# Kernel tuning notes

Hardware: AMD Instinct MI355X
Metric: run time of the kernel (lower is better)

## Reference

```python
import jax, jax.numpy as jnp
import numpy as np

BITS = 4
N_PACK = 8  # 32-bit container / 4-bit values
GROUP_SIZE = 128
MASK = (1 << BITS) - 1  # 0xF


def setup_inputs() -> dict:
    key = jax.random.key(0)
    k1, k2, k3, k4, k5 = jax.random.split(key, 5)
    in_f, out_f = 4096, 4096
    tokens = 8192
    n_groups = in_f // GROUP_SIZE
    x = jax.random.normal(k1, (tokens, in_f), dtype=jnp.float32)
    qweight = jax.random.randint(k2, (in_f // N_PACK, out_f), 0, 2147483647, dtype=jnp.int32)
    qzeros = jax.random.randint(k3, (n_groups, out_f // N_PACK), 0, 2147483647, dtype=jnp.int32)
    scales = jax.random.uniform(k4, (n_groups, out_f), dtype=jnp.float32) * 0.01 + 1e-3
    bias = jax.random.normal(k5, (out_f,), dtype=jnp.float32)
    return {"x": x, "qweight": qweight, "qzeros": qzeros, "scales": scales, "bias": bias}


def _unpack_rows(q):
    # q: [in/8, out] int32 -> [in, out] nibbles (unpack along dim 0)
    shifts = (jnp.arange(N_PACK, dtype=jnp.int32) * BITS)  # [8]
    w = (q[:, None, :] >> shifts[None, :, None]) & MASK    # [in/8, 8, out]
    return w.reshape(-1, q.shape[1])                       # [in, out]


def _unpack_cols(q):
    # q: [G, out/8] int32 -> [G, out] nibbles (unpack along dim 1)
    shifts = (jnp.arange(N_PACK, dtype=jnp.int32) * BITS)
    z = (q[:, :, None] >> shifts[None, None, :]) & MASK    # [G, out/8, 8]
    return z.reshape(q.shape[0], -1)                       # [G, out]


def reference(x, qweight, qzeros, scales, bias):
    in_f = qweight.shape[0] * N_PACK
    int_w = _unpack_rows(qweight)                 # [in, out] uint nibbles
    zp = _unpack_cols(qzeros) + 1                 # optimum format: zp was stored as zp-1
    g = jnp.arange(in_f) // GROUP_SIZE            # group index per input channel
    # dequantize: W[i, j] = (int_w[i,j] - zp[g(i), j]) * scales[g(i), j]
    W = (int_w.astype(jnp.float32) - zp[g].astype(jnp.float32)) * scales[g]
    return x @ W + bias
```

## Files before the change

kernel.cpp:

```cpp
#include <hip/hip_runtime.h>
#include <hip/hip_bf16.h>
#include <stdint.h>

typedef __bf16 bf8 __attribute__((ext_vector_type(8)));
typedef float  f4  __attribute__((ext_vector_type(4)));

__device__ __forceinline__ unsigned f2bf(float f) {
  union { float f; unsigned u; } v; v.f = f;
  return (v.u + 0x7FFFu + ((v.u >> 16) & 1u)) >> 16;
}

__device__ __forceinline__ void gload_lds16(const void* g, void* l) {
  __builtin_amdgcn_global_load_lds(
      (const __attribute__((address_space(1))) void*)(uintptr_t)g,
      (__attribute__((address_space(3))) void*)(uint32_t)(uintptr_t)l,
      16, 0, 0);
}

__global__ void cvt_x(const float4* __restrict__ x, uint4* __restrict__ xb, int n16) {
  int i = blockIdx.x * blockDim.x + threadIdx.x;
  if (i >= n16) return;
  float4 f0 = x[2 * i], f1 = x[2 * i + 1];
  uint4 w;
  w.x = f2bf(f0.x) | (f2bf(f0.y) << 16);
  w.y = f2bf(f0.z) | (f2bf(f0.w) << 16);
  w.z = f2bf(f1.x) | (f2bf(f1.y) << 16);
  w.w = f2bf(f1.z) | (f2bf(f1.w) << 16);
  xb[i] = w;
}

__global__ void dq_w(const int* __restrict__ qw, const int* __restrict__ qz,
                     const float* __restrict__ sc, unsigned short* __restrict__ wt,
                     int N, int K, int group_size) {
  int id = blockIdx.x * blockDim.x + threadIdx.x;
  int n  = id % N;
  int kb = id / N;
  if (kb >= K / 64) return;
  int g = (kb * 64) / group_size;
  unsigned zq = ((unsigned)qz[g * (N >> 3) + (n >> 3)] >> (4 * (n & 7))) & 0xFu;
  float zs = (float)(int)(zq + 1u);
  float s  = sc[(size_t)g * N + n];
  #pragma unroll
  for (int r = 0; r < 8; ++r) {
    unsigned q = (unsigned)qw[(size_t)(kb * 8 + r) * N + n];
    uint4 w;
    #pragma unroll
    for (int h = 0; h < 4; ++h) {
      float v0 = (float)(int)((q >> (8 * h))     & 0xFu) - zs;
      float v1 = (float)(int)((q >> (8 * h + 4)) & 0xFu) - zs;
      ((unsigned*)&w)[h] = f2bf(v0 * s) | (f2bf(v1 * s) << 16);
    }
    *(uint4*)(wt + (size_t)n * K + kb * 64 + r * 8) = w;
  }
}

#define BM 256
#define BN 256
#define BK 64

__launch_bounds__(512, 2)
__global__ void gemm_8ph(const unsigned short* __restrict__ A,
                         const unsigned short* __restrict__ B,
                         const float* __restrict__ bias,
                         float* __restrict__ out,
                         int M, int N, int K) {
  __shared__ __align__(16) char smem[131072];

  const int nbx = N / BN;
  const int nwg = (M / BM) * nbx;
  const int id  = blockIdx.y * gridDim.x + blockIdx.x;
  const int cpx = nwg >> 3;
  const int swzid = (id & 7) * cpx + (id >> 3);
  const int m0 = (swzid / nbx) * BM;
  const int n0 = (swzid % nbx) * BN;

  const int t    = threadIdx.x;
  const int wid  = t >> 6, lane = t & 63;
  const int wr   = wid >> 2, wc = wid & 3;
  const int lr   = lane & 15, lk = lane >> 4;
  const unsigned loff = (unsigned)(lr * 64 + (((lk + (lr >> 1)) & 3) << 4));

  const int srow = lane >> 2;
  const int scol = (((lane & 3) - (lane >> 3)) & 3) * 8;

  f4 acc[8][4] = {};

  const int nK = K / BK;

#define STAGE_A(tile, h)                                                          \
  {                                                                               \
    const int _tt = (tile);                                                       \
    _Pragma("unroll")                                                             \
    for (int cg = 0; cg < 2; ++cg) {                                              \
      const unsigned short* _src = A + (size_t)(m0 + (h) * 128 + wid * 16 + srow) * K \
                                     + _tt * BK + cg * 32 + scol;                 \
      char* _dst = smem + (_tt & 1) * 65536 + ((((h) * 8 + wid) * 2 + cg) << 10); \
      gload_lds16(_src, _dst);                                                    \
    }                                                                             \
  }
#define STAGE_B(tile, h)                                                          \
  {                                                                               \
    const int _tt = (tile);                                                       \
    _Pragma("unroll")                                                             \
    for (int cg = 0; cg < 2; ++cg) {                                              \
      const unsigned short* _src = B + (size_t)(n0 + (h) * 128 + wid * 16 + srow) * K \
                                     + _tt * BK + cg * 32 + scol;                 \
      char* _dst = smem + (_tt & 1) * 65536 + 32768 +                             \
                   ((((h) * 8 + wid) * 2 + cg) << 10);                            \
      gload_lds16(_src, _dst);                                                    \
    }                                                                             \
  }

  STAGE_B(0, 0); STAGE_B(0, 1);
  STAGE_A(0, 0); STAGE_A(0, 1);
  if (nK > 1) {
    STAGE_B(1, 0); STAGE_B(1, 1);
    asm volatile("s_waitcnt vmcnt(4)" ::: "memory");
  } else {
    asm volatile("s_waitcnt vmcnt(0)" ::: "memory");
  }
  __builtin_amdgcn_s_barrier();
  __builtin_amdgcn_sched_barrier(0);

  bf8 a[4][2], b[4][2];

  for (int kt = 0; kt < nK; ++kt) {
    const char* pA = smem + (kt & 1) * 65536;
    const char* pB = pA + 32768;
    const int ra = wr * 8;
    const int rb = wc * 4;

    if (kt + 1 < nK) STAGE_A(kt + 1, 0);
    #pragma unroll
    for (int mf = 0; mf < 4; ++mf)
      #pragma unroll
      for (int ks = 0; ks < 2; ++ks)
        a[mf][ks] = *(const bf8*)(pA + (unsigned)((((ra + mf) * 2 + ks) << 10)) + loff);
    #pragma unroll
    for (int nf = 0; nf < 2; ++nf)
      #pragma unroll
      for (int ks = 0; ks < 2; ++ks)
        b[nf][ks] = *(const bf8*)(pB + (unsigned)((((rb + nf) * 2 + ks) << 10)) + loff);
    __builtin_amdgcn_s_barrier();
    __builtin_amdgcn_s_setprio(1);
    #pragma unroll
    for (int mf = 0; mf < 4; ++mf)
      #pragma unroll
      for (int nf = 0; nf < 2; ++nf)
        #pragma unroll
        for (int ks = 0; ks < 2; ++ks)
          acc[mf][nf] = __builtin_amdgcn_mfma_f32_16x16x32_bf16(a[mf][ks], b[nf][ks], acc[mf][nf], 0, 0, 0);
    __builtin_amdgcn_s_setprio(0);
    __builtin_amdgcn_s_barrier();

    if (kt + 1 < nK) STAGE_A(kt + 1, 1);
    #pragma unroll
    for (int nf = 2; nf < 4; ++nf)
      #pragma unroll
      for (int ks = 0; ks < 2; ++ks)
        b[nf][ks] = *(const bf8*)(pB + (unsigned)((((rb + nf) * 2 + ks) << 10)) + loff);
    __builtin_amdgcn_s_barrier();
    __builtin_amdgcn_s_setprio(1);
    #pragma unroll
    for (int mf = 0; mf < 4; ++mf)
      #pragma unroll
      for (int nf = 2; nf < 4; ++nf)
        #pragma unroll
        for (int ks = 0; ks < 2; ++ks)
          acc[mf][nf] = __builtin_amdgcn_mfma_f32_16x16x32_bf16(a[mf][ks], b[nf][ks], acc[mf][nf], 0, 0, 0);
    __builtin_amdgcn_s_setprio(0);
    __builtin_amdgcn_s_barrier();

    if (kt + 2 < nK) STAGE_B(kt + 2, 0);
    #pragma unroll
    for (int mf = 0; mf < 4; ++mf)
      #pragma unroll
      for (int ks = 0; ks < 2; ++ks)
        a[mf][ks] = *(const bf8*)(pA + (unsigned)((((ra + 4 + mf) * 2 + ks) << 10)) + loff);
    __builtin_amdgcn_s_barrier();
    __builtin_amdgcn_s_setprio(1);
    #pragma unroll
    for (int mf = 0; mf < 4; ++mf)
      #pragma unroll
      for (int nf = 2; nf < 4; ++nf)
        #pragma unroll
        for (int ks = 0; ks < 2; ++ks)
          acc[4 + mf][nf] = __builtin_amdgcn_mfma_f32_16x16x32_bf16(a[mf][ks], b[nf][ks], acc[4 + mf][nf], 0, 0, 0);
    __builtin_amdgcn_s_setprio(0);
    __builtin_amdgcn_s_barrier();

    if (kt + 2 < nK) {
      STAGE_B(kt + 2, 1);
      asm volatile("s_waitcnt vmcnt(4)" ::: "memory");
    } else {
      asm volatile("s_waitcnt vmcnt(0)" ::: "memory");
    }
    __builtin_amdgcn_s_barrier();
    __builtin_amdgcn_sched_barrier(0);
    __builtin_amdgcn_s_setprio(1);
    #pragma unroll
    for (int mf = 0; mf < 4; ++mf)
      #pragma unroll
      for (int nf = 0; nf < 2; ++nf)
        #pragma unroll
        for (int ks = 0; ks < 2; ++ks)
          acc[4 + mf][nf] = __builtin_amdgcn_mfma_f32_16x16x32_bf16(a[mf][ks], b[nf][ks], acc[4 + mf][nf], 0, 0, 0);
    __builtin_amdgcn_s_setprio(0);
    __builtin_amdgcn_s_barrier();
  }

  #pragma unroll
  for (int ni = 0; ni < 4; ++ni) {
    int col = n0 + wc * 64 + ni * 16 + lr;
    float bv = bias[col];
    #pragma unroll
    for (int mi = 0; mi < 8; ++mi) {
      int row = m0 + wr * 128 + mi * 16 + lk * 4;
      #pragma unroll
      for (int r = 0; r < 4; ++r)
        out[(size_t)(row + r) * N + col] = acc[mi][ni][r] + bv;
    }
  }
#undef STAGE_A
#undef STAGE_B
}

#define FBM 128
#define FBN 128
#define FBK 64
__launch_bounds__(256, 2)
__global__ void woq_gemm(const float* __restrict__ x,
                         const int*   __restrict__ qweight,
                         const int*   __restrict__ qzeros,
                         const float* __restrict__ scales,
                         const float* __restrict__ bias,
                         float*       __restrict__ out,
                         int M, int N, int K) {
  __shared__ unsigned short sA[FBM * FBK];
  __shared__ unsigned short sB[FBN * FBK];
  const int t = threadIdx.x;
  const int n0 = blockIdx.x * FBN, m0 = blockIdx.y * FBM;
  const int wid = t >> 6, lane = t & 63;
  const int wr = wid >> 1, wc = wid & 1;
  const int lr = lane & 15, lk = lane >> 4;
  f4 acc[4][4] = {};
  const int c = t & 127, rbase = t >> 7;
  const int segA = t & 7, rowbA = t >> 3;
  const int nK = K / FBK;
  for (int kt = 0; kt < nK; ++kt) {
    const int k0 = kt * FBK;
    __syncthreads();
    #pragma unroll
    for (int p = 0; p < 4; ++p) {
      int row = rowbA + p * 32;
      const float4* src = (const float4*)(x + (size_t)(m0 + row) * K + k0 + segA * 8);
      float4 f0 = src[0], f1 = src[1];
      uint4 w;
      w.x = f2bf(f0.x) | (f2bf(f0.y) << 16);
      w.y = f2bf(f0.z) | (f2bf(f0.w) << 16);
      w.z = f2bf(f1.x) | (f2bf(f1.y) << 16);
      w.w = f2bf(f1.z) | (f2bf(f1.w) << 16);
      unsigned off = (unsigned)(row * (FBK * 2) + segA * 16) ^ ((row & 7) << 4);
      *(uint4*)((char*)sA + off) = w;
    }
    {
      const int g = k0 >> 7;
      const unsigned zq = (unsigned)qzeros[g * (N >> 3) + ((n0 + c) >> 3)];
      const int   zp = (int)((zq >> (4 * ((n0 + c) & 7))) & 0xFu) + 1;
      const float sc = scales[(size_t)g * N + n0 + c];
      #pragma unroll
      for (int p = 0; p < 4; ++p) {
        int r = rbase + p * 2;
        unsigned uq = (unsigned)qweight[(size_t)(kt * 8 + r) * N + n0 + c];
        uint4 w;
        #pragma unroll
        for (int h = 0; h < 4; ++h) {
          int v0 = (int)((uq >> (8 * h))     & 0xFu) - zp;
          int v1 = (int)((uq >> (8 * h + 4)) & 0xFu) - zp;
          ((unsigned*)&w)[h] = f2bf((float)v0 * sc) | (f2bf((float)v1 * sc) << 16);
        }
        unsigned off = (unsigned)(c * (FBK * 2) + r * 16) ^ ((c & 7) << 4);
        *(uint4*)((char*)sB + off) = w;
      }
    }
    __syncthreads();
    #pragma unroll
    for (int ks = 0; ks < 2; ++ks) {
      bf8 a[4], b[4];
      #pragma unroll
      for (int mi = 0; mi < 4; ++mi) {
        int row = wr * 64 + mi * 16 + lr;
        unsigned off = (unsigned)(row * (FBK * 2) + ks * 64 + lk * 16) ^ ((row & 7) << 4);
        a[mi] = *(const bf8*)((const char*)sA + off);
      }
      #pragma unroll
      for (int ni = 0; ni < 4; ++ni) {
        int rowN = wc * 64 + ni * 16 + lr;
        unsigned off = (unsigned)(rowN * (FBK * 2) + ks * 64 + lk * 16) ^ ((rowN & 7) << 4);
        b[ni] = *(const bf8*)((const char*)sB + off);
      }
      #pragma unroll
      for (int mi = 0; mi < 4; ++mi)
        #pragma unroll
        for (int ni = 0; ni < 4; ++ni)
          acc[mi][ni] = __builtin_amdgcn_mfma_f32_16x16x32_bf16(a[mi], b[ni], acc[mi][ni], 0, 0, 0);
    }
  }
  #pragma unroll
  for (int ni = 0; ni < 4; ++ni) {
    int col = n0 + wc * 64 + ni * 16 + lr;
    float bv = bias[col];
    #pragma unroll
    for (int mi = 0; mi < 4; ++mi) {
      int row = m0 + wr * 64 + mi * 16 + lk * 4;
      #pragma unroll
      for (int r = 0; r < 4; ++r)
        out[(size_t)(row + r) * N + col] = acc[mi][ni][r] + bv;
    }
  }
}

extern "C" void kernel_launch(void* const* d_in, const int* in_sizes, int n_in,
                              void* d_out, int out_size, void* d_ws, size_t ws_size,
                              hipStream_t stream) {
  const float* x  = (const float*)d_in[0];
  const int*   qw = (const int*)d_in[1];
  const int*   qz = (const int*)d_in[2];
  const float* sc = (const float*)d_in[3];
  const float* bs = (const float*)d_in[4];
  float* out = (float*)d_out;

  const int N = in_sizes[4];
  const int K = (int)(((long long)in_sizes[1] * 8) / N);
  const int M = (int)((long long)in_sizes[0] / K);
  const int n_groups   = (int)((long long)in_sizes[3] / N);
  const int group_size = K / n_groups;

  const size_t need = ((size_t)M * K + (size_t)N * K) * 2;
  if (ws_size >= need && (M % BM) == 0 && (N % BN) == 0 && (K % BK) == 0 &&
      ((M / BM) * (N / BN)) % 8 == 0) {
    unsigned short* xb = (unsigned short*)d_ws;
    unsigned short* wt = xb + (size_t)M * K;

    int n16 = M * K / 8;
    cvt_x<<<(n16 + 255) / 256, 256, 0, stream>>>((const float4*)x, (uint4*)xb, n16);

    int ndq = N * (K / 64);
    dq_w<<<(ndq + 255) / 256, 256, 0, stream>>>(qw, qz, sc, wt, N, K, group_size);

    dim3 grid(N / BN, M / BM);
    gemm_8ph<<<grid, 512, 0, stream>>>(xb, wt, bs, out, M, N, K);
  } else {
    dim3 grid(N / FBN, M / FBM);
    woq_gemm<<<grid, 256, 0, stream>>>(x, qw, qz, sc, bs, out, M, N, K);
  }
}
```

Before: 301.6 us.

## Replace 8-wave phased GEMM with 4-wave kernel using 128x128 per-wave tiles

The 256x256 GEMM drops from 8 waves with a multi-phase interleaved schedule to 4 waves, each computing a 128x128 sub-tile with 64 accumulators. The loop becomes a simple double-buffered prefetch of the whole next tile followed by a full waitcnt and barrier, with no setprio. The goal is higher per-wave data reuse and fewer barriers. In exchange it gives up the fine-grained load/compute interleaving and runs one 256-thread block per CU with heavy register pressure, which may expose memory latency.

```diff
diff --git a/kernel.cpp b/kernel.cpp
--- a/kernel.cpp
+++ b/kernel.cpp
@@ -58,12 +58,12 @@
 #define BN 256
 #define BK 64
 
-__launch_bounds__(512, 2)
-__global__ void gemm_8ph(const unsigned short* __restrict__ A,
-                         const unsigned short* __restrict__ B,
-                         const float* __restrict__ bias,
-                         float* __restrict__ out,
-                         int M, int N, int K) {
+__launch_bounds__(256, 1)
+__global__ void gemm_4w(const unsigned short* __restrict__ A,
+                        const unsigned short* __restrict__ B,
+                        const float* __restrict__ bias,
+                        float* __restrict__ out,
+                        int M, int N, int K) {
   __shared__ __align__(16) char smem[131072];
 
   const int nbx = N / BN;
@@ -76,153 +76,97 @@
 
   const int t    = threadIdx.x;
   const int wid  = t >> 6, lane = t & 63;
-  const int wr   = wid >> 2, wc = wid & 3;
+  const int wr   = wid >> 1, wc = wid & 1;
   const int lr   = lane & 15, lk = lane >> 4;
   const unsigned loff = (unsigned)(lr * 64 + (((lk + (lr >> 1)) & 3) << 4));
 
   const int srow = lane >> 2;
   const int scol = (((lane & 3) - (lane >> 3)) & 3) * 8;
 
-  f4 acc[8][4] = {};
+  f4 acc[8][8] = {};
 
   const int nK = K / BK;
-
-#define STAGE_A(tile, h)                                                          \
+  const int ra = wr * 8;
+  const int rb = wc * 8;
+
+#define STAGE_A(tile)                                                             \
   {                                                                               \
     const int _tt = (tile);                                                       \
     _Pragma("unroll")                                                             \
-    for (int cg = 0; cg < 2; ++cg) {                                              \
-      const unsigned short* _src = A + (size_t)(m0 + (h) * 128 + wid * 16 + srow) * K \
-                                     + _tt * BK + cg * 32 + scol;                 \
-      char* _dst = smem + (_tt & 1) * 65536 + ((((h) * 8 + wid) * 2 + cg) << 10); \
-      gload_lds16(_src, _dst);                                                    \
+    for (int sg = 0; sg < 4; ++sg) {                                              \
+      _Pragma("unroll")                                                           \
+      for (int cg = 0; cg < 2; ++cg) {                                            \
+        const unsigned short* _src = A + (size_t)(m0 + (wid * 4 + sg) * 16 + srow) * K \
+                                       + _tt * BK + cg * 32 + scol;               \
+        char* _dst = smem + (_tt & 1) * 65536 + (((wid * 4 + sg) * 2 + cg) << 10);\
+        gload_lds16(_src, _dst);                                                  \
+      }                                                                           \
     }                                                                             \
   }
-#define STAGE_B(tile, h)                                                          \
+#define STAGE_B(tile)                                                             \
   {                                                                               \
     const int _tt = (tile);                                                       \
     _Pragma("unroll")                                                             \
-    for (int cg = 0; cg < 2; ++cg) {                                              \
-      const unsigned short* _src = B + (size_t)(n0 + (h) * 128 + wid * 16 + srow) * K \
-                                     + _tt * BK + cg * 32 + scol;                 \
-      char* _dst = smem + (_tt & 1) * 65536 + 32768 +                             \
-                   ((((h) * 8 + wid) * 2 + cg) << 10);                            \
-      gload_lds16(_src, _dst);                                                    \
+    for (int sg = 0; sg < 4; ++sg) {                                              \
+      _Pragma("unroll")                                                           \
+      for (int cg = 0; cg < 2; ++cg) {                                            \
+        const unsigned short* _src = B + (size_t)(n0 + (wid * 4 + sg) * 16 + srow) * K \
+                                       + _tt * BK + cg * 32 + scol;               \
+        char* _dst = smem + (_tt & 1) * 65536 + 32768 +                           \
+                     (((wid * 4 + sg) * 2 + cg) << 10);                           \
+        gload_lds16(_src, _dst);                                                  \
+      }                                                                           \
     }                                                                             \
   }
-
-  STAGE_B(0, 0); STAGE_B(0, 1);
-  STAGE_A(0, 0); STAGE_A(0, 1);
-  if (nK > 1) {
-    STAGE_B(1, 0); STAGE_B(1, 1);
-    asm volatile("s_waitcnt vmcnt(4)" ::: "memory");
-  } else {
-    asm volatile("s_waitcnt vmcnt(0)" ::: "memory");
-  }
+#define RD(p, slot) (*(const bf8*)((p) + ((unsigned)(slot) << 10) + loff))
+
+  STAGE_A(0); STAGE_B(0);
+  asm volatile("s_waitcnt vmcnt(0)" ::: "memory");
   __builtin_amdgcn_s_barrier();
   __builtin_amdgcn_sched_barrier(0);
-
-  bf8 a[4][2], b[4][2];
 
   for (int kt = 0; kt < nK; ++kt) {
     const char* pA = smem + (kt & 1) * 65536;
     const char* pB = pA + 32768;
-    const int ra = wr * 8;
-    const int rb = wc * 4;
-
-    if (kt + 1 < nK) STAGE_A(kt + 1, 0);
-    #pragma unroll
-    for (int mf = 0; mf < 4; ++mf)
-      #pragma unroll
-      for (int ks = 0; ks < 2; ++ks)
-        a[mf][ks] = *(const bf8*)(pA + (unsigned)((((ra + mf) * 2 + ks) << 10)) + loff);
-    #pragma unroll
-    for (int nf = 0; nf < 2; ++nf)
-      #pragma unroll
-      for (int ks = 0; ks < 2; ++ks)
-        b[nf][ks] = *(const bf8*)(pB + (unsigned)((((rb + nf) * 2 + ks) << 10)) + loff);
-    __builtin_amdgcn_s_barrier();
-    __builtin_amdgcn_s_setprio(1);
-    #pragma unroll
-    for (int mf = 0; mf < 4; ++mf)
-      #pragma unroll
-      for (int nf = 0; nf < 2; ++nf)
+
+    if (kt + 1 < nK) { STAGE_A(kt + 1); STAGE_B(kt + 1); }
+
+    #pragma unroll
+    for (int ks = 0; ks < 2; ++ks) {
+      bf8 a[8], b[8];
+      #pragma unroll
+      for (int mi = 0; mi < 8; ++mi)
+        a[mi] = RD(pA, (ra + mi) * 2 + ks);
+      #pragma unroll
+      for (int nj = 0; nj < 8; ++nj)
+        b[nj] = RD(pB, (rb + nj) * 2 + ks);
+      #pragma unroll
+      for (int mi = 0; mi < 8; ++mi)
         #pragma unroll
-        for (int ks = 0; ks < 2; ++ks)
-          acc[mf][nf] = __builtin_amdgcn_mfma_f32_16x16x32_bf16(a[mf][ks], b[nf][ks], acc[mf][nf], 0, 0, 0);
-    __builtin_amdgcn_s_setprio(0);
-    __builtin_amdgcn_s_barrier();
-
-    if (kt + 1 < nK) STAGE_A(kt + 1, 1);
-    #pragma unroll
-    for (int nf = 2; nf < 4; ++nf)
-      #pragma unroll
-      for (int ks = 0; ks < 2; ++ks)
-        b[nf][ks] = *(const bf8*)(pB + (unsigned)((((rb + nf) * 2 + ks) << 10)) + loff);
-    __builtin_amdgcn_s_barrier();
-    __builtin_amdgcn_s_setprio(1);
-    #pragma unroll
-    for (int mf = 0; mf < 4; ++mf)
-      #pragma unroll
-      for (int nf = 2; nf < 4; ++nf)
-        #pragma unroll
-        for (int ks = 0; ks < 2; ++ks)
-          acc[mf][nf] = __builtin_amdgcn_mfma_f32_16x16x32_bf16(a[mf][ks], b[nf][ks], acc[mf][nf], 0, 0, 0);
-    __builtin_amdgcn_s_setprio(0);
-    __builtin_amdgcn_s_barrier();
-
-    if (kt + 2 < nK) STAGE_B(kt + 2, 0);
-    #pragma unroll
-    for (int mf = 0; mf < 4; ++mf)
-      #pragma unroll
-      for (int ks = 0; ks < 2; ++ks)
-        a[mf][ks] = *(const bf8*)(pA + (unsigned)((((ra + 4 + mf) * 2 + ks) << 10)) + loff);
-    __builtin_amdgcn_s_barrier();
-    __builtin_amdgcn_s_setprio(1);
-    #pragma unroll
-    for (int mf = 0; mf < 4; ++mf)
-      #pragma unroll
-      for (int nf = 2; nf < 4; ++nf)
-        #pragma unroll
-        for (int ks = 0; ks < 2; ++ks)
-          acc[4 + mf][nf] = __builtin_amdgcn_mfma_f32_16x16x32_bf16(a[mf][ks], b[nf][ks], acc[4 + mf][nf], 0, 0, 0);
-    __builtin_amdgcn_s_setprio(0);
-    __builtin_amdgcn_s_barrier();
-
-    if (kt + 2 < nK) {
-      STAGE_B(kt + 2, 1);
-      asm volatile("s_waitcnt vmcnt(4)" ::: "memory");
-    } else {
-      asm volatile("s_waitcnt vmcnt(0)" ::: "memory");
-    }
+        for (int nj = 0; nj < 8; ++nj)
+          acc[mi][nj] = __builtin_amdgcn_mfma_f32_16x16x32_bf16(a[mi], b[nj], acc[mi][nj], 0, 0, 0);
+    }
+
+    asm volatile("s_waitcnt vmcnt(0)" ::: "memory");
     __builtin_amdgcn_s_barrier();
     __builtin_amdgcn_sched_barrier(0);
-    __builtin_amdgcn_s_setprio(1);
-    #pragma unroll
-    for (int mf = 0; mf < 4; ++mf)
-      #pragma unroll
-      for (int nf = 0; nf < 2; ++nf)
-        #pragma unroll
-        for (int ks = 0; ks < 2; ++ks)
-          acc[4 + mf][nf] = __builtin_amdgcn_mfma_f32_16x16x32_bf16(a[mf][ks], b[nf][ks], acc[4 + mf][nf], 0, 0, 0);
-    __builtin_amdgcn_s_setprio(0);
-    __builtin_amdgcn_s_barrier();
   }
 
   #pragma unroll
-  for (int ni = 0; ni < 4; ++ni) {
-    int col = n0 + wc * 64 + ni * 16 + lr;
+  for (int nj = 0; nj < 8; ++nj) {
+    int col = n0 + wc * 128 + nj * 16 + lr;
     float bv = bias[col];
     #pragma unroll
     for (int mi = 0; mi < 8; ++mi) {
       int row = m0 + wr * 128 + mi * 16 + lk * 4;
       #pragma unroll
       for (int r = 0; r < 4; ++r)
-        out[(size_t)(row + r) * N + col] = acc[mi][ni][r] + bv;
+        out[(size_t)(row + r) * N + col] = acc[mi][nj][r] + bv;
     }
   }
 #undef STAGE_A
 #undef STAGE_B
+#undef RD
 }
 
 #define FBM 128
@@ -267,7 +211,7 @@
       const int g = k0 >> 7;
       const unsigned zq = (unsigned)qzeros[g * (N >> 3) + ((n0 + c) >> 3)];
       const int   zp = (int)((zq >> (4 * ((n0 + c) & 7))) & 0xFu) + 1;
-      const float sc = scales[(size_t)g * N + n0 + c];
+      const float sc2 = scales[(size_t)g * N + n0 + c];
       #pragma unroll
       for (int p = 0; p < 4; ++p) {
         int r = rbase + p * 2;
@@ -277,7 +221,7 @@
         for (int h = 0; h < 4; ++h) {
           int v0 = (int)((uq >> (8 * h))     & 0xFu) - zp;
           int v1 = (int)((uq >> (8 * h + 4)) & 0xFu) - zp;
-          ((unsigned*)&w)[h] = f2bf((float)v0 * sc) | (f2bf((float)v1 * sc) << 16);
+          ((unsigned*)&w)[h] = f2bf((float)v0 * sc2) | (f2bf((float)v1 * sc2) << 16);
         }
         unsigned off = (unsigned)(c * (FBK * 2) + r * 16) ^ ((c & 7) << 4);
         *(uint4*)((char*)sB + off) = w;
@@ -349,7 +293,7 @@
     dq_w<<<(ndq + 255) / 256, 256, 0, stream>>>(qw, qz, sc, wt, N, K, group_size);
 
     dim3 grid(N / BN, M / BM);
-    gemm_8ph<<<grid, 512, 0, stream>>>(xb, wt, bs, out, M, N, K);
+    gemm_4w<<<grid, 256, 0, stream>>>(xb, wt, bs, out, M, N, K);
   } else {
     dim3 grid(N / FBN, M / FBM);
     woq_gemm<<<grid, 256, 0, stream>>>(x, qw, qz, sc, bs, out, M, N, K);
```

Result: slower. 319.6 us (+5.9%).
